# Kernel optimization log

Hardware: AMD Instinct MI355X
Metric: run time of the kernel (lower is better)

Reference implementation:

```python
import jax, jax.numpy as jnp
import numpy as np

N = 50000        # nodes
E = 800000       # edges (avg degree 16)
F_IN = 256       # cfg.dataset.features
H = 256          # cfg.model.hidden_size


def setup_inputs() -> dict:
    key = jax.random.key(0)
    ks = jax.random.split(key, 8)
    x = jax.random.normal(ks[0], (N, F_IN), dtype=jnp.float32)
    edge_index = jax.random.randint(ks[1], (2, E), 0, N, dtype=jnp.int32)
    # GCNConv weights: layer0 in->hidden, layer1 hidden->hidden, layer2 hidden->1
    W0 = jax.random.normal(ks[2], (F_IN, H), jnp.float32) / np.sqrt(F_IN)
    b0 = jnp.zeros((H,), jnp.float32)
    W1 = jax.random.normal(ks[3], (H, H), jnp.float32) / np.sqrt(H)
    b1 = jnp.zeros((H,), jnp.float32)
    W2 = jax.random.normal(ks[4], (H, 1), jnp.float32) / np.sqrt(H)
    b2 = jnp.zeros((1,), jnp.float32)
    return {"x": x, "edge_index": edge_index, "W0": W0, "b0": b0,
            "W1": W1, "b1": b1, "W2": W2, "b2": b2}


def reference(x, edge_index, W0, b0, W1, b1, W2, b2):
    n = x.shape[0]
    loop = jnp.arange(n, dtype=edge_index.dtype)
    # gcn_norm with self-loops: Ahat = D^{-1/2} (A + I) D^{-1/2}
    src = jnp.concatenate([edge_index[0], loop])  # [E+N]
    dst = jnp.concatenate([edge_index[1], loop])  # [E+N]
    deg = jax.ops.segment_sum(jnp.ones_like(src, dtype=x.dtype), dst, num_segments=n)
    dinv = jnp.where(deg > 0, jax.lax.rsqrt(deg), 0.0)
    norm = dinv[src] * dinv[dst]                  # [E+N]

    def gcn_layer(h, W, b):
        h = h @ W                                              # [N, out]
        agg = jax.ops.segment_sum(norm[:, None] * h[src], dst, num_segments=n)
        return agg + b

    h = jax.nn.relu(gcn_layer(x, W0, b0))
    h = jax.nn.relu(gcn_layer(h, W1, b1))
    return gcn_layer(h, W2, b2)                                # [N, 1]
```

## Files before the change

kernel.cpp:

```cpp
#include <hip/hip_runtime.h>


static inline size_t alignup(size_t x, size_t a) { return (x + a - 1) & ~(a - 1); }

typedef __attribute__((ext_vector_type(8))) short short8;
typedef __attribute__((ext_vector_type(4))) float f32x4;

__device__ inline unsigned short f2bf(float f) {
    union { float f; unsigned int u; } v; v.f = f;
    unsigned int r = v.u + 0x7FFFu + ((v.u >> 16) & 1u);
    return (unsigned short)(r >> 16);
}
__device__ inline float bf2f(unsigned short u) {
    union { unsigned int u; float f; } v; v.u = ((unsigned int)u) << 16;
    return v.f;
}

__global__ __launch_bounds__(256) void k_fill_i32(int* __restrict__ p, int v, int n) {
    int i = blockIdx.x * 256 + threadIdx.x;
    if (i < n) p[i] = v;
}

__global__ __launch_bounds__(256) void k_count_deg(const int* __restrict__ dst, int* __restrict__ deg, int E) {
    int e = blockIdx.x * 256 + threadIdx.x;
    if (e < E) atomicAdd(&deg[dst[e]], 1);
}

__global__ __launch_bounds__(256) void k_scan1(const int* __restrict__ deg, int* __restrict__ rs,
                                               int* __restrict__ bsum, float* __restrict__ dinv, int n) {
    __shared__ int sd[256];
    int b = blockIdx.x, tid = threadIdx.x;
    int base = b * 1024 + tid * 4;
    int v[4];
#pragma unroll
    for (int j = 0; j < 4; ++j) v[j] = (base + j < n) ? deg[base + j] : 0;
    int tot = v[0] + v[1] + v[2] + v[3];
    sd[tid] = tot;
    for (int off = 1; off < 256; off <<= 1) {
        __syncthreads();
        int t = (tid >= off) ? sd[tid - off] : 0;
        __syncthreads();
        sd[tid] += t;
    }
    __syncthreads();
    int run = tid ? sd[tid - 1] : 0;
#pragma unroll
    for (int j = 0; j < 4; ++j) {
        if (base + j < n) {
            rs[base + j] = run;
            dinv[base + j] = rsqrtf((float)v[j] + 1.0f);
        }
        run += v[j];
    }
    if (tid == 255) bsum[b] = sd[255];
}

__global__ __launch_bounds__(256) void k_scan2(int* __restrict__ bsum, int nb) {
    __shared__ int sd[256];
    int tid = threadIdx.x;
    sd[tid] = (tid < nb) ? bsum[tid] : 0;
    for (int off = 1; off < 256; off <<= 1) {
        __syncthreads();
        int t = (tid >= off) ? sd[tid - off] : 0;
        __syncthreads();
        sd[tid] += t;
    }
    __syncthreads();
    if (tid < nb) bsum[tid] = tid ? sd[tid - 1] : 0;
}

__global__ __launch_bounds__(256) void k_scan3(int* __restrict__ rs, int* __restrict__ cursor,
                                               const int* __restrict__ bsum, int n, int E) {
    int b = blockIdx.x, tid = threadIdx.x;
    int off = bsum[b];
    int base = b * 1024 + tid * 4;
#pragma unroll
    for (int j = 0; j < 4; ++j) {
        int idx = base + j;
        if (idx < n) {
            int v = rs[idx] + off;
            rs[idx] = v;
            cursor[idx] = v;
        }
    }
    if (b == 0 && tid == 0) rs[n] = E;
}

__global__ __launch_bounds__(256) void k_fill_csr(const int* __restrict__ src, const int* __restrict__ dst,
                                                  int* __restrict__ cursor, int* __restrict__ col, int E) {
    int e = blockIdx.x * 256 + threadIdx.x;
    if (e < E) {
        int d = dst[e];
        int pos = atomicAdd(&cursor[d], 1);
        col[pos] = src[e];
    }
}

__global__ __launch_bounds__(256) void k_wt2(const float* __restrict__ W0, const float* __restrict__ W1,
                                             unsigned short* __restrict__ Wt0, unsigned short* __restrict__ Wt1) {
    int idx = blockIdx.x * 256 + threadIdx.x;
    const float* W = (idx < 65536) ? W0 : W1;
    unsigned short* Wt = (idx < 65536) ? Wt0 : Wt1;
    int id = idx & 65535;
    int k = id >> 8, n = id & 255;
    Wt[(size_t)n * 256 + k] = f2bf(W[(size_t)k * 256 + n]);
}

template <bool AF32>
__global__ __launch_bounds__(256) void k_gemm_mfma(const void* __restrict__ Ap,
                                                   const unsigned short* __restrict__ Wt,
                                                   unsigned short* __restrict__ C,
                                                   const float* __restrict__ dinv, int N) {
    __shared__ __align__(16) unsigned short smem[16384];
    unsigned short* Asb[2] = {smem, smem + 8192};
    unsigned short* Bsb[2] = {smem + 4096, smem + 12288};
    unsigned short* Cs = smem;

    int tid = threadIdx.x;
    int lane = tid & 63, w = tid >> 6;
    int wr = w >> 1, wc = w & 1;
    int row0 = blockIdx.y * 128, col0 = blockIdx.x * 128;

    f32x4 acc[4][4];
#pragma unroll
    for (int m = 0; m < 4; ++m)
#pragma unroll
        for (int n = 0; n < 4; ++n) acc[m][n] = (f32x4)0.f;

    const int c0 = tid, c1 = tid + 256;
    const int ar0 = c0 >> 2, akg0 = c0 & 3, ar1 = c1 >> 2, akg1 = c1 & 3;

    auto loadA = [&](int r, int kg, int k0) -> short8 {
        short8 u = {0, 0, 0, 0, 0, 0, 0, 0};
        int grow = row0 + r;
        if (grow < N) {
            if constexpr (AF32) {
                const float* g = (const float*)Ap + (size_t)grow * 256 + k0 + kg * 8;
                float4 f0 = *(const float4*)g;
                float4 f1 = *(const float4*)(g + 4);
                u[0] = (short)f2bf(f0.x); u[1] = (short)f2bf(f0.y);
                u[2] = (short)f2bf(f0.z); u[3] = (short)f2bf(f0.w);
                u[4] = (short)f2bf(f1.x); u[5] = (short)f2bf(f1.y);
                u[6] = (short)f2bf(f1.z); u[7] = (short)f2bf(f1.w);
            } else {
                u = *(const short8*)((const unsigned short*)Ap + (size_t)grow * 256 + k0 + kg * 8);
            }
        }
        return u;
    };
    auto loadB = [&](int n, int kg, int k0) -> short8 {
        return *(const short8*)(Wt + (size_t)(col0 + n) * 256 + k0 + kg * 8);
    };
    auto stash = [&](int buf, short8 a0, short8 a1, short8 b0, short8 b1) {
        *(short8*)&Asb[buf][(ar0 >> 4) * 512 + akg0 * 128 + (ar0 & 15) * 8] = a0;
        *(short8*)&Asb[buf][(ar1 >> 4) * 512 + akg1 * 128 + (ar1 & 15) * 8] = a1;
        *(short8*)&Bsb[buf][(ar0 >> 4) * 512 + akg0 * 128 + (ar0 & 15) * 8] = b0;
        *(short8*)&Bsb[buf][(ar1 >> 4) * 512 + akg1 * 128 + (ar1 & 15) * 8] = b1;
    };

    {
        short8 a0 = loadA(ar0, akg0, 0), a1 = loadA(ar1, akg1, 0);
        short8 b0 = loadB(ar0, akg0, 0), b1 = loadB(ar1, akg1, 0);
        stash(0, a0, a1, b0, b1);
    }
    __syncthreads();

#pragma unroll
    for (int i = 0; i < 8; ++i) {
        int cur = i & 1;
        short8 na0, na1, nb0, nb1;
        if (i < 7) {
            int k0 = i * 32 + 32;
            na0 = loadA(ar0, akg0, k0); na1 = loadA(ar1, akg1, k0);
            nb0 = loadB(ar0, akg0, k0); nb1 = loadB(ar1, akg1, k0);
        }
        short8 af[4], bfr[4];
#pragma unroll
        for (int m = 0; m < 4; ++m)
            af[m] = *(const short8*)&Asb[cur][(wr * 4 + m) * 512 + (lane >> 4) * 128 + (lane & 15) * 8];
#pragma unroll
        for (int n = 0; n < 4; ++n)
            bfr[n] = *(const short8*)&Bsb[cur][(wc * 4 + n) * 512 + (lane >> 4) * 128 + (lane & 15) * 8];
#pragma unroll
        for (int m = 0; m < 4; ++m)
#pragma unroll
            for (int n = 0; n < 4; ++n)
                acc[m][n] = __builtin_amdgcn_mfma_f32_16x16x32_bf16(af[m], bfr[n], acc[m][n], 0, 0, 0);
        if (i < 7) stash(cur ^ 1, na0, na1, nb0, nb1);
        __syncthreads();
    }

    unsigned short* myCs = &Cs[w * 4096];
#pragma unroll
    for (int m = 0; m < 4; ++m) {
#pragma unroll
        for (int j = 0; j < 4; ++j) {
            int r = m * 16 + (lane >> 4) * 4 + j;
            int grow = row0 + wr * 64 + r;
            float d = (grow < N) ? dinv[grow] : 0.f;
#pragma unroll
            for (int n = 0; n < 4; ++n)
                myCs[r * 64 + n * 16 + (lane & 15)] = f2bf(acc[m][n][j] * d);
        }
    }
    __syncthreads();
#pragma unroll
    for (int i = 0; i < 8; ++i) {
        int r = i * 8 + (lane >> 3);
        int grow = row0 + wr * 64 + r;
        if (grow < N) {
            short8 v = *(const short8*)&myCs[r * 64 + (lane & 7) * 8];
            *(short8*)(C + (size_t)grow * 256 + col0 + wc * 64 + (lane & 7) * 8) = v;
        }
    }
}

template <bool FUSE_GEMV>
__global__ __launch_bounds__(256) void k_agg(const unsigned short* __restrict__ t,
                                             unsigned short* __restrict__ h,
                                             const int* __restrict__ rs, const int* __restrict__ col,
                                             const float* __restrict__ dinv, const float* __restrict__ bias,
                                             const float* __restrict__ W2, float* __restrict__ z,
                                             int N) {
    int wid = (blockIdx.x * 256 + threadIdx.x) >> 6;
    int lane = threadIdx.x & 63;
    if (wid >= N) return;
    int half = lane >> 5, sub = lane & 31;
    const short8* tp = (const short8*)t;

    short8 sv = tp[(size_t)wid * 32 + sub];
    float hsel = (half == 0) ? 1.f : 0.f;
    float a[8];
#pragma unroll
    for (int i = 0; i < 8; ++i) a[i] = hsel * bf2f((unsigned short)sv[i]);

    int e0 = rs[wid], e1 = rs[wid + 1];
    for (int base = e0; base < e1; base += 64) {
        int m = e1 - base; if (m > 64) m = 64;
        int c = (base + lane < e1) ? col[base + lane] : 0;
        int npairs = (m + 1) >> 1;
        int j = 0;
        for (; j + 4 <= npairs; j += 4) {
            int i0 = 2 * j + half, i1 = i0 + 2, i2 = i0 + 4, i3 = i0 + 6;
            int s0 = __shfl(c, i0), s1 = __shfl(c, i1), s2 = __shfl(c, i2), s3 = __shfl(c, i3);
            float f0 = (i0 < m) ? 1.f : 0.f, f1 = (i1 < m) ? 1.f : 0.f;
            float f2 = (i2 < m) ? 1.f : 0.f, f3 = (i3 < m) ? 1.f : 0.f;
            short8 w0 = tp[(size_t)s0 * 32 + sub];
            short8 w1 = tp[(size_t)s1 * 32 + sub];
            short8 w2 = tp[(size_t)s2 * 32 + sub];
            short8 w3 = tp[(size_t)s3 * 32 + sub];
#pragma unroll
            for (int i = 0; i < 8; ++i) {
                a[i] = fmaf(f0, bf2f((unsigned short)w0[i]), a[i]);
                a[i] = fmaf(f1, bf2f((unsigned short)w1[i]), a[i]);
                a[i] = fmaf(f2, bf2f((unsigned short)w2[i]), a[i]);
                a[i] = fmaf(f3, bf2f((unsigned short)w3[i]), a[i]);
            }
        }
        for (; j < npairs; ++j) {
            int i0 = 2 * j + half;
            int s0 = __shfl(c, i0);
            float f0 = (i0 < m) ? 1.f : 0.f;
            short8 w0 = tp[(size_t)s0 * 32 + sub];
#pragma unroll
            for (int i = 0; i < 8; ++i) a[i] = fmaf(f0, bf2f((unsigned short)w0[i]), a[i]);
        }
    }
#pragma unroll
    for (int i = 0; i < 8; ++i) a[i] += __shfl_xor(a[i], 32, 64);

    float d = dinv[wid];
    float4 b0 = ((const float4*)bias)[sub * 2];
    float4 b1 = ((const float4*)bias)[sub * 2 + 1];
    float o[8];
    o[0] = fmaf(d, a[0], b0.x); o[1] = fmaf(d, a[1], b0.y);
    o[2] = fmaf(d, a[2], b0.z); o[3] = fmaf(d, a[3], b0.w);
    o[4] = fmaf(d, a[4], b1.x); o[5] = fmaf(d, a[5], b1.y);
    o[6] = fmaf(d, a[6], b1.z); o[7] = fmaf(d, a[7], b1.w);
#pragma unroll
    for (int i = 0; i < 8; ++i) o[i] = fmaxf(o[i], 0.f);

    if constexpr (FUSE_GEMV) {
        float4 wv0 = ((const float4*)W2)[sub * 2];
        float4 wv1 = ((const float4*)W2)[sub * 2 + 1];
        float zp = o[0] * wv0.x + o[1] * wv0.y + o[2] * wv0.z + o[3] * wv0.w +
                   o[4] * wv1.x + o[5] * wv1.y + o[6] * wv1.z + o[7] * wv1.w;
#pragma unroll
        for (int off = 16; off > 0; off >>= 1) zp += __shfl_down(zp, off, 32);
        if (lane == 0) z[wid] = d * zp;
    } else {
        if (half == 0) {
            short8 u;
#pragma unroll
            for (int i = 0; i < 8; ++i) u[i] = (short)f2bf(o[i]);
            *(short8*)(h + (size_t)wid * 256 + sub * 8) = u;
        }
    }
}

__global__ __launch_bounds__(256) void k_agg_out(const float* __restrict__ z, float* __restrict__ out,
                                                 const int* __restrict__ rs, const int* __restrict__ col,
                                                 const float* __restrict__ dinv, const float* __restrict__ b2,
                                                 int N) {
    int wid = (blockIdx.x * 256 + threadIdx.x) >> 6;
    int lane = threadIdx.x & 63;
    if (wid >= N) return;
    int e0 = rs[wid], e1 = rs[wid + 1];
    float v = 0.f;
    for (int base = e0; base < e1; base += 64) {
        int e = base + lane;
        if (e < e1) v += z[col[e]];
    }
#pragma unroll
    for (int off = 32; off > 0; off >>= 1) v += __shfl_down(v, off, 64);
    if (lane == 0) out[wid] = fmaf(dinv[wid], v + z[wid], b2[0]);
}

extern "C" void kernel_launch(void* const* d_in, const int* in_sizes, int n_in,
                              void* d_out, int out_size, void* d_ws, size_t ws_size,
                              hipStream_t stream) {
    const float* x  = (const float*)d_in[0];
    const int*   ei = (const int*)d_in[1];
    const float* W0 = (const float*)d_in[2];
    const float* b0 = (const float*)d_in[3];
    const float* W1 = (const float*)d_in[4];
    const float* b1 = (const float*)d_in[5];
    const float* W2 = (const float*)d_in[6];
    const float* b2 = (const float*)d_in[7];
    float* out = (float*)d_out;

    int N = in_sizes[0] / 256;
    int E = in_sizes[1] / 2;
    const int* esrc = ei;
    const int* edst = ei + E;

    char* p = (char*)d_ws;
    unsigned short* tb = (unsigned short*)p; p += alignup((size_t)N * 256 * 2, 16);
    unsigned short* hb = (unsigned short*)p; p += alignup((size_t)N * 256 * 2, 16);
    unsigned short* Wt0 = (unsigned short*)p; p += 256 * 256 * 2;
    unsigned short* Wt1 = (unsigned short*)p; p += 256 * 256 * 2;
    float* z = (float*)p;      p += alignup((size_t)N * 4, 16);
    float* dinv = (float*)p;   p += alignup((size_t)N * 4, 16);
    int* deg = (int*)p;        p += alignup((size_t)N * 4, 16);
    int* cursor = (int*)p;     p += alignup((size_t)N * 4, 16);
    int* rs = (int*)p;         p += alignup((size_t)(N + 1) * 4, 16);
    int* col = (int*)p;        p += alignup((size_t)E * 4, 16);
    int* bsum = (int*)p;       p += 256 * 4;

    int nb = (N + 1023) / 1024;
    dim3 blk(256);

    k_fill_i32<<<(N + 255) / 256, blk, 0, stream>>>(deg, 0, N);
    k_count_deg<<<(E + 255) / 256, blk, 0, stream>>>(edst, deg, E);
    k_scan1<<<nb, blk, 0, stream>>>(deg, rs, bsum, dinv, N);
    k_scan2<<<1, blk, 0, stream>>>(bsum, nb);
    k_scan3<<<nb, blk, 0, stream>>>(rs, cursor, bsum, N, E);
    k_fill_csr<<<(E + 255) / 256, blk, 0, stream>>>(esrc, edst, cursor, col, E);
    k_wt2<<<512, blk, 0, stream>>>(W0, W1, Wt0, Wt1);

    dim3 gg(2, (N + 127) / 128);
    k_gemm_mfma<true><<<gg, blk, 0, stream>>>(x, Wt0, tb, dinv, N);
    k_agg<false><<<(N + 3) / 4, blk, 0, stream>>>(tb, hb, rs, col, dinv, b0, nullptr, nullptr, N);
    k_gemm_mfma<false><<<gg, blk, 0, stream>>>(hb, Wt1, tb, dinv, N);
    k_agg<true><<<(N + 3) / 4, blk, 0, stream>>>(tb, nullptr, rs, col, dinv, b1, W2, z, N);
    k_agg_out<<<(N + 3) / 4, blk, 0, stream>>>(z, out, rs, col, dinv, b2, N);
}
```

Measured before the change: 370.0 us.

## Fuse setup kernels, merge scan passes, load GEMM B fragments directly from global

Merges the degree zero-fill with the weight transpose into one init kernel, and folds the single-block block-sum scan into the final scan kernel, where each block redundantly rescans the block sums. The GEMM no longer stages W tiles through LDS; each wave loads its B fragments straight from global (L2-resident weights) into registers, double-buffered across k-steps, and each thread loads A with wider per-thread chunks. This cuts launch count and LDS traffic and barrier work, at the cost of more registers and redundant global B reads across waves.

```diff
diff --git a/kernel.cpp b/kernel.cpp
--- a/kernel.cpp
+++ b/kernel.cpp
@@ -16,9 +16,22 @@
     return v.f;
 }
 
-__global__ __launch_bounds__(256) void k_fill_i32(int* __restrict__ p, int v, int n) {
-    int i = blockIdx.x * 256 + threadIdx.x;
-    if (i < n) p[i] = v;
+__global__ __launch_bounds__(256) void k_init(int* __restrict__ deg, int n, int nbN,
+                                              const float* __restrict__ W0, const float* __restrict__ W1,
+                                              unsigned short* __restrict__ Wt0,
+                                              unsigned short* __restrict__ Wt1) {
+    int b = blockIdx.x;
+    if (b < nbN) {
+        int i = b * 256 + threadIdx.x;
+        if (i < n) deg[i] = 0;
+    } else {
+        int idx = (b - nbN) * 256 + threadIdx.x;
+        const float* W = (idx < 65536) ? W0 : W1;
+        unsigned short* Wt = (idx < 65536) ? Wt0 : Wt1;
+        int id = idx & 65535;
+        int k = id >> 8, nn = id & 255;
+        Wt[(size_t)nn * 256 + k] = f2bf(W[(size_t)k * 256 + nn]);
+    }
 }
 
 __global__ __launch_bounds__(256) void k_count_deg(const int* __restrict__ dst, int* __restrict__ deg, int E) {
@@ -55,9 +68,10 @@
     if (tid == 255) bsum[b] = sd[255];
 }
 
-__global__ __launch_bounds__(256) void k_scan2(int* __restrict__ bsum, int nb) {
+__global__ __launch_bounds__(256) void k_scan3(int* __restrict__ rs, int* __restrict__ cursor,
+                                               const int* __restrict__ bsum, int nb, int n, int E) {
     __shared__ int sd[256];
-    int tid = threadIdx.x;
+    int b = blockIdx.x, tid = threadIdx.x;
     sd[tid] = (tid < nb) ? bsum[tid] : 0;
     for (int off = 1; off < 256; off <<= 1) {
         __syncthreads();
@@ -66,13 +80,7 @@
         sd[tid] += t;
     }
     __syncthreads();
-    if (tid < nb) bsum[tid] = tid ? sd[tid - 1] : 0;
-}
-
-__global__ __launch_bounds__(256) void k_scan3(int* __restrict__ rs, int* __restrict__ cursor,
-                                               const int* __restrict__ bsum, int n, int E) {
-    int b = blockIdx.x, tid = threadIdx.x;
-    int off = bsum[b];
+    int off = b ? sd[b - 1] : 0;
     int base = b * 1024 + tid * 4;
 #pragma unroll
     for (int j = 0; j < 4; ++j) {
@@ -96,24 +104,13 @@
     }
 }
 
-__global__ __launch_bounds__(256) void k_wt2(const float* __restrict__ W0, const float* __restrict__ W1,
-                                             unsigned short* __restrict__ Wt0, unsigned short* __restrict__ Wt1) {
-    int idx = blockIdx.x * 256 + threadIdx.x;
-    const float* W = (idx < 65536) ? W0 : W1;
-    unsigned short* Wt = (idx < 65536) ? Wt0 : Wt1;
-    int id = idx & 65535;
-    int k = id >> 8, n = id & 255;
-    Wt[(size_t)n * 256 + k] = f2bf(W[(size_t)k * 256 + n]);
-}
-
 template <bool AF32>
 __global__ __launch_bounds__(256) void k_gemm_mfma(const void* __restrict__ Ap,
                                                    const unsigned short* __restrict__ Wt,
                                                    unsigned short* __restrict__ C,
                                                    const float* __restrict__ dinv, int N) {
     __shared__ __align__(16) unsigned short smem[16384];
-    unsigned short* Asb[2] = {smem, smem + 8192};
-    unsigned short* Bsb[2] = {smem + 4096, smem + 12288};
+    unsigned short* Asb[2] = {smem, smem + 4096};
     unsigned short* Cs = smem;
 
     int tid = threadIdx.x;
@@ -127,66 +124,75 @@
 #pragma unroll
         for (int n = 0; n < 4; ++n) acc[m][n] = (f32x4)0.f;
 
-    const int c0 = tid, c1 = tid + 256;
-    const int ar0 = c0 >> 2, akg0 = c0 & 3, ar1 = c1 >> 2, akg1 = c1 & 3;
-
-    auto loadA = [&](int r, int kg, int k0) -> short8 {
-        short8 u = {0, 0, 0, 0, 0, 0, 0, 0};
-        int grow = row0 + r;
+    const int ar = tid >> 1, akg = (tid & 1) << 1;
+    const unsigned short* Bbase = Wt + (size_t)(col0 + wc * 64 + (lane & 15)) * 256 + (lane >> 4) * 8;
+
+    auto loadA2 = [&](int k0, short8& u0, short8& u1) {
+        u0 = (short8){0, 0, 0, 0, 0, 0, 0, 0}; u1 = u0;
+        int grow = row0 + ar;
         if (grow < N) {
             if constexpr (AF32) {
-                const float* g = (const float*)Ap + (size_t)grow * 256 + k0 + kg * 8;
+                const float* g = (const float*)Ap + (size_t)grow * 256 + k0 + akg * 8;
                 float4 f0 = *(const float4*)g;
                 float4 f1 = *(const float4*)(g + 4);
-                u[0] = (short)f2bf(f0.x); u[1] = (short)f2bf(f0.y);
-                u[2] = (short)f2bf(f0.z); u[3] = (short)f2bf(f0.w);
-                u[4] = (short)f2bf(f1.x); u[5] = (short)f2bf(f1.y);
-                u[6] = (short)f2bf(f1.z); u[7] = (short)f2bf(f1.w);
+                float4 f2 = *(const float4*)(g + 8);
+                float4 f3 = *(const float4*)(g + 12);
+                u0[0] = (short)f2bf(f0.x); u0[1] = (short)f2bf(f0.y);
+                u0[2] = (short)f2bf(f0.z); u0[3] = (short)f2bf(f0.w);
+                u0[4] = (short)f2bf(f1.x); u0[5] = (short)f2bf(f1.y);
+                u0[6] = (short)f2bf(f1.z); u0[7] = (short)f2bf(f1.w);
+                u1[0] = (short)f2bf(f2.x); u1[1] = (short)f2bf(f2.y);
+                u1[2] = (short)f2bf(f2.z); u1[3] = (short)f2bf(f2.w);
+                u1[4] = (short)f2bf(f3.x); u1[5] = (short)f2bf(f3.y);
+                u1[6] = (short)f2bf(f3.z); u1[7] = (short)f2bf(f3.w);
             } else {
-                u = *(const short8*)((const unsigned short*)Ap + (size_t)grow * 256 + k0 + kg * 8);
+                const unsigned short* g = (const unsigned short*)Ap + (size_t)grow * 256 + k0 + akg * 8;
+                u0 = *(const short8*)g;
+                u1 = *(const short8*)(g + 8);
             }
         }
-        return u;
     };
-    auto loadB = [&](int n, int kg, int k0) -> short8 {
-        return *(const short8*)(Wt + (size_t)(col0 + n) * 256 + k0 + kg * 8);
+    auto stashA = [&](int buf, short8 u0, short8 u1) {
+        *(short8*)&Asb[buf][(ar >> 4) * 512 + akg * 128 + (ar & 15) * 8] = u0;
+        *(short8*)&Asb[buf][(ar >> 4) * 512 + (akg + 1) * 128 + (ar & 15) * 8] = u1;
     };
-    auto stash = [&](int buf, short8 a0, short8 a1, short8 b0, short8 b1) {
-        *(short8*)&Asb[buf][(ar0 >> 4) * 512 + akg0 * 128 + (ar0 & 15) * 8] = a0;
-        *(short8*)&Asb[buf][(ar1 >> 4) * 512 + akg1 * 128 + (ar1 & 15) * 8] = a1;
-        *(short8*)&Bsb[buf][(ar0 >> 4) * 512 + akg0 * 128 + (ar0 & 15) * 8] = b0;
-        *(short8*)&Bsb[buf][(ar1 >> 4) * 512 + akg1 * 128 + (ar1 & 15) * 8] = b1;
+    auto loadBfrags = [&](int k0, short8* bf) {
+#pragma unroll
+        for (int n = 0; n < 4; ++n)
+            bf[n] = *(const short8*)(Bbase + (size_t)(n * 16) * 256 + k0);
     };
 
+    short8 bcur[4], bnext[4];
     {
-        short8 a0 = loadA(ar0, akg0, 0), a1 = loadA(ar1, akg1, 0);
-        short8 b0 = loadB(ar0, akg0, 0), b1 = loadB(ar1, akg1, 0);
-        stash(0, a0, a1, b0, b1);
+        short8 a0, a1;
+        loadA2(0, a0, a1);
+        stashA(0, a0, a1);
+        loadBfrags(0, bcur);
     }
     __syncthreads();
 
 #pragma unroll
     for (int i = 0; i < 8; ++i) {
         int cur = i & 1;
-        short8 na0, na1, nb0, nb1;
+        short8 na0, na1;
         if (i < 7) {
-            int k0 = i * 32 + 32;
-            na0 = loadA(ar0, akg0, k0); na1 = loadA(ar1, akg1, k0);
-            nb0 = loadB(ar0, akg0, k0); nb1 = loadB(ar1, akg1, k0);
-        }
-        short8 af[4], bfr[4];
+            loadA2(i * 32 + 32, na0, na1);
+            loadBfrags(i * 32 + 32, bnext);
+        }
+        short8 af[4];
 #pragma unroll
         for (int m = 0; m < 4; ++m)
             af[m] = *(const short8*)&Asb[cur][(wr * 4 + m) * 512 + (lane >> 4) * 128 + (lane & 15) * 8];
 #pragma unroll
-        for (int n = 0; n < 4; ++n)
-            bfr[n] = *(const short8*)&Bsb[cur][(wc * 4 + n) * 512 + (lane >> 4) * 128 + (lane & 15) * 8];
-#pragma unroll
         for (int m = 0; m < 4; ++m)
 #pragma unroll
             for (int n = 0; n < 4; ++n)
-                acc[m][n] = __builtin_amdgcn_mfma_f32_16x16x32_bf16(af[m], bfr[n], acc[m][n], 0, 0, 0);
-        if (i < 7) stash(cur ^ 1, na0, na1, nb0, nb1);
+                acc[m][n] = __builtin_amdgcn_mfma_f32_16x16x32_bf16(af[m], bcur[n], acc[m][n], 0, 0, 0);
+        if (i < 7) {
+            stashA(cur ^ 1, na0, na1);
+#pragma unroll
+            for (int n = 0; n < 4; ++n) bcur[n] = bnext[n];
+        }
         __syncthreads();
     }
 
@@ -348,15 +354,14 @@
     int* bsum = (int*)p;       p += 256 * 4;
 
     int nb = (N + 1023) / 1024;
+    int nbN = (N + 255) / 256;
     dim3 blk(256);
 
-    k_fill_i32<<<(N + 255) / 256, blk, 0, stream>>>(deg, 0, N);
+    k_init<<<nbN + 512, blk, 0, stream>>>(deg, N, nbN, W0, W1, Wt0, Wt1);
     k_count_deg<<<(E + 255) / 256, blk, 0, stream>>>(edst, deg, E);
     k_scan1<<<nb, blk, 0, stream>>>(deg, rs, bsum, dinv, N);
-    k_scan2<<<1, blk, 0, stream>>>(bsum, nb);
-    k_scan3<<<nb, blk, 0, stream>>>(rs, cursor, bsum, N, E);
+    k_scan3<<<nb, blk, 0, stream>>>(rs, cursor, bsum, nb, N, E);
     k_fill_csr<<<(E + 255) / 256, blk, 0, stream>>>(esrc, edst, cursor, col, E);
-    k_wt2<<<512, blk, 0, stream>>>(W0, W1, Wt0, Wt1);
 
     dim3 gg(2, (N + 127) / 128);
     k_gemm_mfma<true><<<gg, blk, 0, stream>>>(x, Wt0, tb, dinv, N);
```

Result: no change. 364.0 us (-1.6%).
